# Performance work log

Hardware: AMD Instinct MI355X
Metric: run time of the kernel (lower is better)

The kernel has to match this reference:

```python
import jax, jax.numpy as jnp
import numpy as np

D_MODEL = 512
H = 8
DH = D_MODEL // H
P = H * (H - 1) // 2  # 28 head pairs
THRESH = 0.1
B, N = 2, 2048

# pair indices (i<j) in the same row-major order as the nested torch loop
_I_IDX, _J_IDX = np.triu_indices(H, k=1)
I_IDX = jnp.asarray(_I_IDX)
J_IDX = jnp.asarray(_J_IDX)


def setup_inputs() -> dict:
    key = jax.random.key(0)
    ks = jax.random.split(key, 10)
    s = 1.0 / np.sqrt(D_MODEL)
    return {
        "x": jax.random.normal(ks[0], (B, N, D_MODEL), dtype=jnp.float32),
        "Wq": jax.random.normal(ks[1], (D_MODEL, D_MODEL), dtype=jnp.float32) * s,
        "bq": jnp.zeros((D_MODEL,), dtype=jnp.float32),
        "Wk": jax.random.normal(ks[2], (D_MODEL, D_MODEL), dtype=jnp.float32) * s,
        "bk": jnp.zeros((D_MODEL,), dtype=jnp.float32),
        "Wv": jax.random.normal(ks[3], (D_MODEL, D_MODEL), dtype=jnp.float32) * s,
        "bv": jnp.zeros((D_MODEL,), dtype=jnp.float32),
        "Wo": jax.random.normal(ks[4], (D_MODEL, D_MODEL), dtype=jnp.float32) * s,
        "bo": jnp.zeros((D_MODEL,), dtype=jnp.float32),
        # stacked restriction maps: (P, DH_out, DH_in), Linear(bias=False)
        "Wr": jax.random.normal(ks[5], (P, DH, DH), dtype=jnp.float32) / np.sqrt(DH),
        "agreement_scale": jnp.asarray(1.0, dtype=jnp.float32),
    }


def reference(x, Wq, bq, Wk, bk, Wv, bv, Wo, bo, Wr, agreement_scale):
    b, n, d = x.shape
    # projections (torch Linear: y = x @ W.T + b), split into heads -> (B,H,N,DH)
    q = (x @ Wq.T + bq).reshape(b, n, H, DH).transpose(0, 2, 1, 3)
    k = (x @ Wk.T + bk).reshape(b, n, H, DH).transpose(0, 2, 1, 3)
    v = (x @ Wv.T + bv).reshape(b, n, H, DH).transpose(0, 2, 1, 3)

    scores = jnp.einsum("bhnd,bhmd->bhnm", q, k) / jnp.sqrt(jnp.asarray(DH, x.dtype))
    attn = jax.nn.softmax(scores, axis=-1)
    head_out = jnp.einsum("bhnm,bhmd->bhnd", attn, v)  # (B,H,N,DH)

    # --- pairwise restriction-map agreement, fully batched over the P pairs ---
    hi = head_out[:, I_IDX]  # (B,P,N,DH)
    hj = head_out[:, J_IDX]  # (B,P,N,DH)
    ri = jnp.einsum("bpnd,ped->bpne", hi, Wr)  # per-pair Linear(bias=False)
    diff = jnp.linalg.norm(ri - hj, axis=-1).mean(axis=-1)  # (B,P)
    score = jnp.exp(-diff * agreement_scale / THRESH)  # (B,P)

    agreement = jnp.zeros((b, H, H), dtype=x.dtype)
    agreement = agreement.at[:, I_IDX, J_IDX].set(score)
    agreement = agreement.at[:, J_IDX, I_IDX].set(score)
    diag = jnp.arange(H)
    agreement = agreement.at[:, diag, diag].set(1.0)

    # --- consensus aggregation ---
    offdiag = 1.0 - jnp.eye(H, dtype=x.dtype)
    consensus = (agreement * offdiag).sum(axis=-1) / (H - 1)  # (B,H)
    filtered = consensus * (consensus > THRESH).astype(x.dtype)
    weights = jax.nn.softmax(filtered + 1e-10, axis=-1)  # (B,H)

    agg = (head_out * weights[:, :, None, None]).sum(axis=1)  # (B,N,DH)
    agg = jnp.tile(agg, (1, 1, H))  # torch .repeat(1,1,H) -> (B,N,D)
    return agg @ Wo.T + bo
```

## Files before the change

### kernel.cpp

```cpp
#include <hip/hip_runtime.h>
#include <hip/hip_bf16.h>
#include <stdint.h>

typedef __attribute__((ext_vector_type(8))) short bf16x8;
typedef __attribute__((ext_vector_type(4))) float f32x4;
typedef __attribute__((ext_vector_type(4))) unsigned short u16x4;

#define LDS_SWZ(row, col) (((((col) >> 3) ^ ((row) & 7)) << 4))

__device__ __forceinline__ unsigned short f2bf(float f) {
  union { float f; unsigned u; } v; v.f = f;
  unsigned r = v.u + 0x7FFFu + ((v.u >> 16) & 1u);
  return (unsigned short)(r >> 16);
}
__device__ __forceinline__ float bf2f(unsigned short h) {
  union { unsigned u; float f; } v; v.u = ((unsigned)h) << 16;
  return v.f;
}
__device__ __forceinline__ unsigned pk2bf(float a, float b) {
  __hip_bfloat162 h2 = __float22bfloat162_rn(float2{a, b});
  unsigned u; __builtin_memcpy(&u, &h2, 4); return u;
}
__device__ __forceinline__ void gld_lds16(const void* g, void* l) {
  __builtin_amdgcn_global_load_lds((const __attribute__((address_space(1))) void*)g,
                                   (__attribute__((address_space(3))) void*)l, 16, 0, 0);
}

__global__ void k_prep(const float* __restrict__ x, const float* __restrict__ wq,
                       const float* __restrict__ wk, const float* __restrict__ wv,
                       const float* __restrict__ wr, const float* __restrict__ wo,
                       unsigned short* __restrict__ xb, unsigned short* __restrict__ wb,
                       unsigned short* __restrict__ wrb, unsigned short* __restrict__ wsb) {
  int q = blockIdx.x * blockDim.x + threadIdx.x;
  if (q >= 749568) {
    int t = q - 749568;
    if (t >= 512 * 64) return;
    int e = t >> 6, d = t & 63;
    float s = 0.f;
#pragma unroll
    for (int qq = 0; qq < 8; ++qq) s += wo[e * 512 + qq * 64 + d];
    wsb[t] = f2bf(s);
    return;
  }
  const float* src; unsigned short* dst; int off;
  if (q < 524288)      { src = x;  dst = xb;          off = q; }
  else if (q < 589824) { src = wq; dst = wb;          off = q - 524288; }
  else if (q < 655360) { src = wk; dst = wb + 262144; off = q - 589824; }
  else if (q < 720896) { src = wv; dst = wb + 524288; off = q - 655360; }
  else                 { src = wr; dst = wrb;         off = q - 720896; }
  float4 v = ((const float4*)src)[off];
  u16x4 o; o.x = f2bf(v.x); o.y = f2bf(v.y); o.z = f2bf(v.z); o.w = f2bf(v.w);
  ((u16x4*)dst)[off] = o;
}

__global__ __launch_bounds__(256) void k_qkv(
    const unsigned short* __restrict__ xb, const unsigned short* __restrict__ wb,
    const float* __restrict__ bq, const float* __restrict__ bk, const float* __restrict__ bv,
    unsigned short* __restrict__ qb, unsigned short* __restrict__ kb,
    unsigned short* __restrict__ vtb) {
  __shared__ alignas(16) unsigned char As[2][128 * 128];
  __shared__ alignas(16) unsigned char Bs[2][64 * 128];
  const int tid = threadIdx.x;
  const int wave = tid >> 6, lane = tid & 63;
  const int rowbase = blockIdx.x * 128;
  const int colbase = blockIdx.y * 64;
  const int z = blockIdx.z;
  const unsigned short* W = wb + z * 512 * 512;
  const float* bias = (z == 0) ? bq : ((z == 1) ? bk : bv);
  f32x4 acc[2][4] = {};

#define QKV_STAGE(buf, kt_)                                                            \
  do {                                                                                 \
    _Pragma("unroll") for (int i_ = 0; i_ < 4; ++i_) {                                 \
      const int L_ = i_ * 256 + tid;                                                   \
      const int row_ = L_ >> 3, pos_ = L_ & 7;                                         \
      gld_lds16(xb + (rowbase + row_) * 512 + (kt_) * 64 + ((pos_ ^ (row_ & 7)) << 3), \
                As[buf] + (i_ * 256 + wave * 64) * 16);                                \
    }                                                                                  \
    _Pragma("unroll") for (int i_ = 0; i_ < 2; ++i_) {                                 \
      const int L_ = i_ * 256 + tid;                                                   \
      const int row_ = L_ >> 3, pos_ = L_ & 7;                                         \
      gld_lds16(W + (colbase + row_) * 512 + (kt_) * 64 + ((pos_ ^ (row_ & 7)) << 3),  \
                Bs[buf] + (i_ * 256 + wave * 64) * 16);                                \
    }                                                                                  \
  } while (0)

  QKV_STAGE(0, 0);
  __syncthreads();
  for (int kt = 0; kt < 8; ++kt) {
    const int cur = kt & 1;
    if (kt < 7) QKV_STAGE(cur ^ 1, kt + 1);
#pragma unroll
    for (int kc = 0; kc < 2; ++kc) {
      bf16x8 af[2], bfr[4];
#pragma unroll
      for (int mq = 0; mq < 2; ++mq) {
        const int row = wave * 32 + mq * 16 + (lane & 15);
        const int col = kc * 32 + ((lane >> 4) << 3);
        af[mq] = *(const bf16x8*)(As[cur] + row * 128 + LDS_SWZ(row, col));
      }
#pragma unroll
      for (int nq = 0; nq < 4; ++nq) {
        const int row = nq * 16 + (lane & 15);
        const int col = kc * 32 + ((lane >> 4) << 3);
        bfr[nq] = *(const bf16x8*)(Bs[cur] + row * 128 + LDS_SWZ(row, col));
      }
#pragma unroll
      for (int mq = 0; mq < 2; ++mq)
#pragma unroll
        for (int nq = 0; nq < 4; ++nq)
          acc[mq][nq] = __builtin_amdgcn_mfma_f32_16x16x32_bf16(af[mq], bfr[nq], acc[mq][nq], 0, 0, 0);
    }
    __syncthreads();
  }
  const float qs = 0.18033688011112043f;
#pragma unroll
  for (int mq = 0; mq < 2; ++mq)
#pragma unroll
    for (int nq = 0; nq < 4; ++nq)
#pragma unroll
      for (int r = 0; r < 4; ++r) {
        const int grow = rowbase + wave * 32 + mq * 16 + ((lane >> 4) << 2) + r;
        const int col = colbase + nq * 16 + (lane & 15);
        float v = acc[mq][nq][r] + bias[col];
        const int b = grow >> 11, n = grow & 2047;
        const int h = col >> 6, dh = col & 63;
        if (z == 0)      qb[(((b << 3) + h) * 2048 + n) * 64 + dh] = f2bf(v * qs);
        else if (z == 1) kb[(((b << 3) + h) * 2048 + n) * 64 + dh] = f2bf(v);
        else             vtb[((((b << 3) + h) << 6) + dh) * 2048 + n] = f2bf(v);
      }
}

__global__ __launch_bounds__(512, 4) void k_attn(
    const unsigned short* __restrict__ qb, const unsigned short* __restrict__ kb,
    const unsigned short* __restrict__ vtb, unsigned short* __restrict__ hob) {
  __shared__ alignas(16) unsigned char smem[81920];
  const int tid = threadIdx.x, wave = tid >> 6, lane = tid & 63;
  const int team = wave >> 2, w4 = wave & 3;
  const int ttid = tid & 255;
  const int bid = blockIdx.x;
  const int bh = ((bid & 7) << 1) | ((bid >> 3) & 1);
  const int qt = bid >> 4;
  const int n0 = qt * 64 + w4 * 16;
  const int lq = lane & 15, lg = lane >> 4;
  unsigned char* Kt = smem + team * 32768;
  unsigned char* Vt = Kt + 16384;
  unsigned char* pw = smem + 65536 + wave * 2048;
  const unsigned short* kbase = kb + bh * 2048 * 64;
  const unsigned short* vbase = vtb + bh * 64 * 2048;
  bf16x8 qf[2];
#pragma unroll
  for (int kc = 0; kc < 2; ++kc)
    qf[kc] = *(const bf16x8*)(qb + (bh * 2048 + n0 + lq) * 64 + kc * 32 + (lg << 3));
  bf16x8 ones;
#pragma unroll
  for (int e = 0; e < 8; ++e) ones[e] = (short)0x3F80;
  f32x4 oacc[4] = {};
  f32x4 lacc = {};
  float mrun = -1e30f;

#define ATTN_STAGE(buf, T_)                                                        \
  do {                                                                             \
    _Pragma("unroll") for (int i_ = 0; i_ < 2; ++i_) {                             \
      const int L_ = i_ * 256 + ttid;                                              \
      const int row_ = L_ >> 3, pos_ = L_ & 7;                                     \
      gld_lds16(kbase + ((T_) * 64 + row_) * 64 + ((pos_ ^ (row_ & 7)) << 3),      \
                Kt + (buf) * 8192 + (i_ * 256 + w4 * 64) * 16);                    \
      gld_lds16(vbase + row_ * 2048 + (T_) * 64 + ((pos_ ^ (row_ & 7)) << 3),      \
                Vt + (buf) * 8192 + (i_ * 256 + w4 * 64) * 16);                    \
    }                                                                              \
  } while (0)

  ATTN_STAGE(0, team * 16);
  __syncthreads();
  for (int t = 0; t < 16; ++t) {
    const int cur = t & 1;
    if (t < 15) ATTN_STAGE(cur ^ 1, team * 16 + t + 1);
    f32x4 s[4];
    __builtin_amdgcn_s_setprio(1);
#pragma unroll
    for (int mc = 0; mc < 4; ++mc) {
      f32x4 zz = {};
#pragma unroll
      for (int kc = 0; kc < 2; ++kc) {
        const int row = mc * 16 + lq;
        const int col = kc * 32 + (lg << 3);
        bf16x8 kf = *(const bf16x8*)(Kt + cur * 8192 + row * 128 + LDS_SWZ(row, col));
        zz = __builtin_amdgcn_mfma_f32_16x16x32_bf16(kf, qf[kc], zz, 0, 0, 0);
      }
      s[mc] = zz;
    }
    __builtin_amdgcn_s_setprio(0);
    float t0 = fmaxf(fmaxf(s[0][0], s[0][1]), s[0][2]);
    float t1 = fmaxf(fmaxf(s[0][3], s[1][0]), s[1][1]);
    float t2 = fmaxf(fmaxf(s[1][2], s[1][3]), s[2][0]);
    float t3 = fmaxf(fmaxf(s[2][1], s[2][2]), s[2][3]);
    float t4 = fmaxf(fmaxf(s[3][0], s[3][1]), s[3][2]);
    float lm = fmaxf(fmaxf(fmaxf(t0, t1), t2), fmaxf(fmaxf(t3, t4), s[3][3]));
    if (__any(lm > mrun + 8.f)) {
      float v = fmaxf(lm, __shfl_xor(lm, 16));
      v = fmaxf(v, __shfl_xor(v, 32));
      float mnew = fmaxf(mrun, v);
      float sc = exp2f(mrun - mnew);
      mrun = mnew;
      float sco[4];
#pragma unroll
      for (int r = 0; r < 4; ++r) sco[r] = __shfl(sc, (lane & 48) | ((lg << 2) + r));
#pragma unroll
      for (int c2 = 0; c2 < 4; ++c2) {
        f32x4 o = oacc[c2];
#pragma unroll
        for (int r = 0; r < 4; ++r) o[r] *= sco[r];
        oacc[c2] = o;
      }
#pragma unroll
      for (int r = 0; r < 4; ++r) lacc[r] *= sco[r];
    }
#pragma unroll
    for (int mc = 0; mc < 4; ++mc) {
      float p0 = exp2f(s[mc][0] - mrun);
      float p1 = exp2f(s[mc][1] - mrun);
      float p2 = exp2f(s[mc][2] - mrun);
      float p3 = exp2f(s[mc][3] - mrun);
      *(uint2*)(pw + (mc * 4 + lg) * 128 + lq * 8) = uint2{pk2bf(p0, p1), pk2bf(p2, p3)};
    }
    bf16x8 pa[2];
#pragma unroll
    for (int kc = 0; kc < 2; ++kc) {
      uint2 a = *(const uint2*)(pw + (kc * 8 + lg * 2) * 128 + lq * 8);
      uint2 b = *(const uint2*)(pw + (kc * 8 + lg * 2 + 1) * 128 + lq * 8);
      union { uint4 u; bf16x8 v; } cv; cv.u = uint4{a.x, a.y, b.x, b.y};
      pa[kc] = cv.v;
    }
    __builtin_amdgcn_s_setprio(1);
    lacc = __builtin_amdgcn_mfma_f32_16x16x32_bf16(pa[0], ones, lacc, 0, 0, 0);
    lacc = __builtin_amdgcn_mfma_f32_16x16x32_bf16(pa[1], ones, lacc, 0, 0, 0);
#pragma unroll
    for (int c2 = 0; c2 < 4; ++c2) {
      f32x4 o = oacc[c2];
#pragma unroll
      for (int kc = 0; kc < 2; ++kc) {
        const int row = c2 * 16 + lq;
        const int col = kc * 32 + (lg << 3);
        bf16x8 vf = *(const bf16x8*)(Vt + cur * 8192 + row * 128 + LDS_SWZ(row, col));
        o = __builtin_amdgcn_mfma_f32_16x16x32_bf16(pa[kc], vf, o, 0, 0, 0);
      }
      oacc[c2] = o;
    }
    __builtin_amdgcn_s_setprio(0);
    __syncthreads();
  }
  float m_o[4];
#pragma unroll
  for (int r = 0; r < 4; ++r) m_o[r] = __shfl(mrun, (lane & 48) | ((lg << 2) + r));
  float* ex = (float*)smem;
  float* px = ex + (w4 * 64 + lane) * 25;
  if (team == 1) {
#pragma unroll
    for (int c2 = 0; c2 < 4; ++c2)
#pragma unroll
      for (int r = 0; r < 4; ++r) px[c2 * 4 + r] = oacc[c2][r];
#pragma unroll
    for (int r = 0; r < 4; ++r) { px[16 + r] = m_o[r]; px[20 + r] = lacc[r]; }
  }
  __syncthreads();
  if (team == 0) {
    float w0[4], w1[4];
#pragma unroll
    for (int r = 0; r < 4; ++r) {
      float m1 = px[16 + r], l1 = px[20 + r];
      float ms = fmaxf(m_o[r], m1);
      float a = exp2f(m_o[r] - ms), b = exp2f(m1 - ms);
      float li = 1.f / (a * lacc[r] + b * l1);
      w0[r] = a * li; w1[r] = b * li;
    }
#pragma unroll
    for (int c2 = 0; c2 < 4; ++c2)
#pragma unroll
      for (int r = 0; r < 4; ++r) {
        const int n = n0 + (lg << 2) + r;
        const int dh = c2 * 16 + lq;
        float o1 = px[c2 * 4 + r];
        hob[(bh * 2048 + n) * 64 + dh] = f2bf(w0[r] * oacc[c2][r] + w1[r] * o1);
      }
  }
}

__global__ __launch_bounds__(256) void k_pair(const unsigned short* __restrict__ hob,
                                              const unsigned short* __restrict__ wrb,
                                              float* __restrict__ dpart) {
  __shared__ alignas(16) unsigned char Ws[64 * 128];
  __shared__ alignas(16) unsigned char Hj[2][64 * 128];
  __shared__ float red[4];
  const int tid = threadIdx.x, wave = tid >> 6, lane = tid & 63;
  const int chunk = blockIdx.x & 7, bp = blockIdx.x >> 3;
  const int b = bp / 28, p = bp % 28;
  int pp = p, ii = 0;
  while (pp >= 7 - ii) { pp -= 7 - ii; ii++; }
  const int i = ii, j = ii + 1 + pp;
  const unsigned short* hib = hob + ((b * 8 + i) * 2048) * 64;
  const unsigned short* hjb = hob + ((b * 8 + j) * 2048) * 64;

#define PAIR_STAGE(buf, t_)                                                      \
  do {                                                                           \
    _Pragma("unroll") for (int is_ = 0; is_ < 2; ++is_) {                        \
      const int L_ = is_ * 256 + tid;                                            \
      const int row_ = L_ >> 3, pos_ = L_ & 7;                                   \
      gld_lds16(hjb + ((t_) * 64 + row_) * 64 + ((pos_ ^ (row_ & 7)) << 3),      \
                Hj[buf] + (is_ * 256 + wave * 64) * 16);                         \
    }                                                                            \
  } while (0)

#pragma unroll
  for (int is = 0; is < 2; ++is) {
    const int L = is * 256 + tid;
    const int row = L >> 3, pos = L & 7;
    gld_lds16(wrb + (p * 64 + row) * 64 + ((pos ^ (row & 7)) << 3), Ws + (is * 256 + wave * 64) * 16);
  }
  PAIR_STAGE(0, chunk * 4);
  __syncthreads();
  bf16x8 wf[4][2];
#pragma unroll
  for (int c = 0; c < 4; ++c)
#pragma unroll
    for (int kc = 0; kc < 2; ++kc) {
      const int row = c * 16 + (lane & 15);
      const int col = kc * 32 + ((lane >> 4) << 3);
      wf[c][kc] = *(const bf16x8*)(Ws + row * 128 + LDS_SWZ(row, col));
    }
  float wacc = 0.f;
  for (int t = 0; t < 4; ++t) {
    const int tt = chunk * 4 + t;
    const int cur = t & 1;
    if (t < 3) PAIR_STAGE(cur ^ 1, tt + 1);
    const int rbase = tt * 64 + wave * 16;
    f32x4 ri[4] = {};
#pragma unroll
    for (int kc = 0; kc < 2; ++kc) {
      bf16x8 hf = *(const bf16x8*)(hib + (rbase + (lane & 15)) * 64 + kc * 32 + ((lane >> 4) << 3));
#pragma unroll
      for (int c = 0; c < 4; ++c)
        ri[c] = __builtin_amdgcn_mfma_f32_16x16x32_bf16(hf, wf[c][kc], ri[c], 0, 0, 0);
    }
#pragma unroll
    for (int r = 0; r < 4; ++r) {
      const int row = wave * 16 + ((lane >> 4) << 2) + r;
      float ss = 0.f;
#pragma unroll
      for (int c = 0; c < 4; ++c) {
        const int col = c * 16 + (lane & 15);
        float hv = bf2f(*(const unsigned short*)(Hj[cur] + (row & 63) * 128 + LDS_SWZ(row & 63, col) + ((col & 7) << 1)));
        float d = ri[c][r] - hv;
        ss += d * d;
      }
#pragma unroll
      for (int off = 1; off < 16; off <<= 1) ss += __shfl_xor(ss, off);
      if ((lane & 15) == 0) wacc += sqrtf(ss);
    }
    __syncthreads();
  }
  float tot = __shfl(wacc, 0) + __shfl(wacc, 16) + __shfl(wacc, 32) + __shfl(wacc, 48);
  if (lane == 0) red[wave] = tot;
  __syncthreads();
  if (tid == 0) dpart[blockIdx.x] = red[0] + red[1] + red[2] + red[3];
}

__global__ __launch_bounds__(256) void k_agg(const unsigned short* __restrict__ hob,
                                             const float* __restrict__ dpart,
                                             const float* __restrict__ scal,
                                             unsigned short* __restrict__ aggb) {
  __shared__ float sc_s[2][28];
  __shared__ float filt[2][8];
  __shared__ float wts_s[16];
  const int tid = threadIdx.x;
  if (tid < 56) {
    int bb = tid / 28, pp = tid % 28;
    int base = (bb * 28 + pp) * 8;
    float diff = 0.f;
#pragma unroll
    for (int c = 0; c < 8; ++c) diff += dpart[base + c];
    diff /= 2048.f;
    sc_s[bb][pp] = expf(-diff * scal[0] / 0.1f);
  }
  __syncthreads();
  if (tid < 16) {
    int bb = tid / 8, h = tid % 8;
    float cons = 0.f;
    for (int h2 = 0; h2 < 8; ++h2)
      if (h2 != h) {
        int i_ = h < h2 ? h : h2, j_ = h < h2 ? h2 : h;
        int pp = i_ * (15 - i_) / 2 + (j_ - i_ - 1);
        cons += sc_s[bb][pp];
      }
    cons /= 7.f;
    filt[bb][h] = (cons > 0.1f) ? cons : 0.f;
  }
  __syncthreads();
  if (tid < 16) {
    int bb = tid / 8, h = tid % 8;
    float m = -1e30f;
    for (int h2 = 0; h2 < 8; ++h2) m = fmaxf(m, filt[bb][h2] + 1e-10f);
    float s = 0.f;
    for (int h2 = 0; h2 < 8; ++h2) s += expf(filt[bb][h2] + 1e-10f - m);
    wts_s[tid] = expf(filt[bb][h] + 1e-10f - m) / s;
  }
  __syncthreads();
  int t = blockIdx.x * blockDim.x + tid;
  if (t >= 4096 * 8) return;
  int r = t >> 3, dblk = t & 7;
  int b = r >> 11, n = r & 2047;
  float acc[8] = {};
#pragma unroll
  for (int h = 0; h < 8; ++h) {
    float w = wts_s[b * 8 + h];
    bf16x8 v = *(const bf16x8*)(hob + (((b * 8 + h) << 11) + n) * 64 + dblk * 8);
#pragma unroll
    for (int e = 0; e < 8; ++e) acc[e] += w * bf2f((unsigned short)v[e]);
  }
  bf16x8 o;
#pragma unroll
  for (int e = 0; e < 8; ++e) o[e] = (short)f2bf(acc[e]);
  *(bf16x8*)(aggb + r * 64 + dblk * 8) = o;
}

__global__ __launch_bounds__(256) void k_out(const unsigned short* __restrict__ aggb,
                                             const unsigned short* __restrict__ wsb,
                                             const float* __restrict__ bo,
                                             float* __restrict__ out) {
  __shared__ alignas(16) unsigned char Ws[64 * 128];
  const int tid = threadIdx.x, wave = tid >> 6, lane = tid & 63;
  const int rowb = blockIdx.x * 64, colb = blockIdx.y * 64;
#pragma unroll
  for (int is = 0; is < 2; ++is) {
    const int L = is * 256 + tid;
    const int row = L >> 3, pos = L & 7;
    gld_lds16(wsb + (colb + row) * 64 + ((pos ^ (row & 7)) << 3), Ws + (is * 256 + wave * 64) * 16);
  }
  __syncthreads();
  bf16x8 af[2];
#pragma unroll
  for (int kc = 0; kc < 2; ++kc)
    af[kc] = *(const bf16x8*)(aggb + (rowb + wave * 16 + (lane & 15)) * 64 + kc * 32 + ((lane >> 4) << 3));
  f32x4 acc[4] = {};
#pragma unroll
  for (int c = 0; c < 4; ++c)
#pragma unroll
    for (int kc = 0; kc < 2; ++kc) {
      const int row = c * 16 + (lane & 15);
      const int col = kc * 32 + ((lane >> 4) << 3);
      bf16x8 wfr = *(const bf16x8*)(Ws + row * 128 + LDS_SWZ(row, col));
      acc[c] = __builtin_amdgcn_mfma_f32_16x16x32_bf16(af[kc], wfr, acc[c], 0, 0, 0);
    }
#pragma unroll
  for (int c = 0; c < 4; ++c)
#pragma unroll
    for (int r = 0; r < 4; ++r) {
      const int grow = rowb + wave * 16 + ((lane >> 4) << 2) + r;
      const int col = colb + c * 16 + (lane & 15);
      out[grow * 512 + col] = acc[c][r] + bo[col];
    }
}

extern "C" void kernel_launch(void* const* d_in, const int* in_sizes, int n_in,
                              void* d_out, int out_size, void* d_ws, size_t ws_size,
                              hipStream_t stream) {
  const float* x  = (const float*)d_in[0];
  const float* Wq = (const float*)d_in[1];
  const float* bq = (const float*)d_in[2];
  const float* Wk = (const float*)d_in[3];
  const float* bk = (const float*)d_in[4];
  const float* Wv = (const float*)d_in[5];
  const float* bv = (const float*)d_in[6];
  const float* Wo = (const float*)d_in[7];
  const float* bo = (const float*)d_in[8];
  const float* Wr = (const float*)d_in[9];
  const float* ascale = (const float*)d_in[10];
  float* out = (float*)d_out;

  char* ws = (char*)d_ws;
  unsigned short* xb   = (unsigned short*)(ws);
  unsigned short* qb   = (unsigned short*)(ws + (4u << 20));
  unsigned short* kb   = (unsigned short*)(ws + (8u << 20));
  unsigned short* vtb  = (unsigned short*)(ws + (12u << 20));
  unsigned short* hob  = (unsigned short*)(ws + (16u << 20));
  unsigned short* wb   = (unsigned short*)(ws + (20u << 20));
  unsigned short* wrb  = (unsigned short*)(ws + (20u << 20) + 3u * 512 * 512 * 2);
  unsigned short* wsb  = (unsigned short*)(ws + (20u << 20) + 3u * 512 * 512 * 2 + 28u * 64 * 64 * 2);
  unsigned short* aggb = (unsigned short*)(ws + (22u << 20));
  float* dpart = (float*)(ws + (23u << 20));

  k_prep<<<3056, 256, 0, stream>>>(x, Wq, Wk, Wv, Wr, Wo, xb, wb, wrb, wsb);
  k_qkv<<<dim3(32, 8, 3), 256, 0, stream>>>(xb, wb, bq, bk, bv, qb, kb, vtb);
  k_attn<<<512, 512, 0, stream>>>(qb, kb, vtb, hob);
  k_pair<<<448, 256, 0, stream>>>(hob, wrb, dpart);
  k_agg<<<128, 256, 0, stream>>>(hob, dpart, ascale, aggb);
  k_out<<<dim3(64, 8), 256, 0, stream>>>(aggb, wsb, bo, out);
}
```

Measured before the change: 79.51 us.

## Split attention KV range across four waves per 16-query block, read K/V directly

Reworks the attention kernel so each 256-thread block handles 16 queries, with each of its four waves covering a quarter of the key range. K and V fragments are now read straight from global memory instead of being staged through double-buffered LDS, which removes the per-tile barriers. The four partial softmax states are then merged by a two-level tree reduction in shared memory. This adds parallelism and occupancy, but K/V reuse across query rows within a block is lost, so global/L2 traffic rises and loads are no longer overlapped by explicit prefetch.

```diff
diff --git a/kernel.cpp b/kernel.cpp
--- a/kernel.cpp
+++ b/kernel.cpp
@@ -131,21 +131,18 @@
       }
 }
 
-__global__ __launch_bounds__(512, 4) void k_attn(
+__global__ __launch_bounds__(256, 6) void k_attn(
     const unsigned short* __restrict__ qb, const unsigned short* __restrict__ kb,
     const unsigned short* __restrict__ vtb, unsigned short* __restrict__ hob) {
-  __shared__ alignas(16) unsigned char smem[81920];
+  __shared__ alignas(16) unsigned char smem[21504];
   const int tid = threadIdx.x, wave = tid >> 6, lane = tid & 63;
-  const int team = wave >> 2, w4 = wave & 3;
-  const int ttid = tid & 255;
   const int bid = blockIdx.x;
   const int bh = ((bid & 7) << 1) | ((bid >> 3) & 1);
   const int qt = bid >> 4;
-  const int n0 = qt * 64 + w4 * 16;
+  const int n0 = qt * 16;
   const int lq = lane & 15, lg = lane >> 4;
-  unsigned char* Kt = smem + team * 32768;
-  unsigned char* Vt = Kt + 16384;
-  unsigned char* pw = smem + 65536 + wave * 2048;
+  unsigned char* pw = smem + wave * 2048;
+  float* ex = (float*)(smem + 8192);
   const unsigned short* kbase = kb + bh * 2048 * 64;
   const unsigned short* vbase = vtb + bh * 64 * 2048;
   bf16x8 qf[2];
@@ -159,23 +156,10 @@
   f32x4 lacc = {};
   float mrun = -1e30f;
 
-#define ATTN_STAGE(buf, T_)                                                        \
-  do {                                                                             \
-    _Pragma("unroll") for (int i_ = 0; i_ < 2; ++i_) {                             \
-      const int L_ = i_ * 256 + ttid;                                              \
-      const int row_ = L_ >> 3, pos_ = L_ & 7;                                     \
-      gld_lds16(kbase + ((T_) * 64 + row_) * 64 + ((pos_ ^ (row_ & 7)) << 3),      \
-                Kt + (buf) * 8192 + (i_ * 256 + w4 * 64) * 16);                    \
-      gld_lds16(vbase + row_ * 2048 + (T_) * 64 + ((pos_ ^ (row_ & 7)) << 3),      \
-                Vt + (buf) * 8192 + (i_ * 256 + w4 * 64) * 16);                    \
-    }                                                                              \
-  } while (0)
-
-  ATTN_STAGE(0, team * 16);
-  __syncthreads();
-  for (int t = 0; t < 16; ++t) {
-    const int cur = t & 1;
-    if (t < 15) ATTN_STAGE(cur ^ 1, team * 16 + t + 1);
+  for (int t = 0; t < 8; ++t) {
+    const int T = wave * 8 + t;
+    const unsigned short* kt = kbase + T * 64 * 64;
+    const unsigned short* vt = vbase + T * 64;
     f32x4 s[4];
     __builtin_amdgcn_s_setprio(1);
 #pragma unroll
@@ -183,9 +167,7 @@
       f32x4 zz = {};
 #pragma unroll
       for (int kc = 0; kc < 2; ++kc) {
-        const int row = mc * 16 + lq;
-        const int col = kc * 32 + (lg << 3);
-        bf16x8 kf = *(const bf16x8*)(Kt + cur * 8192 + row * 128 + LDS_SWZ(row, col));
+        bf16x8 kf = *(const bf16x8*)(kt + (mc * 16 + lq) * 64 + kc * 32 + (lg << 3));
         zz = __builtin_amdgcn_mfma_f32_16x16x32_bf16(kf, qf[kc], zz, 0, 0, 0);
       }
       s[mc] = zz;
@@ -240,22 +222,18 @@
       f32x4 o = oacc[c2];
 #pragma unroll
       for (int kc = 0; kc < 2; ++kc) {
-        const int row = c2 * 16 + lq;
-        const int col = kc * 32 + (lg << 3);
-        bf16x8 vf = *(const bf16x8*)(Vt + cur * 8192 + row * 128 + LDS_SWZ(row, col));
+        bf16x8 vf = *(const bf16x8*)(vt + (c2 * 16 + lq) * 2048 + kc * 32 + (lg << 3));
         o = __builtin_amdgcn_mfma_f32_16x16x32_bf16(pa[kc], vf, o, 0, 0, 0);
       }
       oacc[c2] = o;
     }
     __builtin_amdgcn_s_setprio(0);
-    __syncthreads();
   }
   float m_o[4];
 #pragma unroll
   for (int r = 0; r < 4; ++r) m_o[r] = __shfl(mrun, (lane & 48) | ((lg << 2) + r));
-  float* ex = (float*)smem;
-  float* px = ex + (w4 * 64 + lane) * 25;
-  if (team == 1) {
+  if (wave & 1) {
+    float* px = ex + ((wave >> 1) * 64 + lane) * 25;
 #pragma unroll
     for (int c2 = 0; c2 < 4; ++c2)
 #pragma unroll
@@ -264,16 +242,46 @@
     for (int r = 0; r < 4; ++r) { px[16 + r] = m_o[r]; px[20 + r] = lacc[r]; }
   }
   __syncthreads();
-  if (team == 0) {
-    float w0[4], w1[4];
+  if (!(wave & 1)) {
+    float* px = ex + ((wave >> 1) * 64 + lane) * 25;
+    float aa[4], bb[4];
 #pragma unroll
     for (int r = 0; r < 4; ++r) {
       float m1 = px[16 + r], l1 = px[20 + r];
       float ms = fmaxf(m_o[r], m1);
-      float a = exp2f(m_o[r] - ms), b = exp2f(m1 - ms);
-      float li = 1.f / (a * lacc[r] + b * l1);
-      w0[r] = a * li; w1[r] = b * li;
-    }
+      aa[r] = exp2f(m_o[r] - ms); bb[r] = exp2f(m1 - ms);
+      m_o[r] = ms; lacc[r] = aa[r] * lacc[r] + bb[r] * l1;
+    }
+#pragma unroll
+    for (int c2 = 0; c2 < 4; ++c2)
+#pragma unroll
+      for (int r = 0; r < 4; ++r)
+        oacc[c2][r] = aa[r] * oacc[c2][r] + bb[r] * px[c2 * 4 + r];
+  }
+  __syncthreads();
+  if (wave == 2) {
+    float* px = ex + lane * 25;
+#pragma unroll
+    for (int c2 = 0; c2 < 4; ++c2)
+#pragma unroll
+      for (int r = 0; r < 4; ++r) px[c2 * 4 + r] = oacc[c2][r];
+#pragma unroll
+    for (int r = 0; r < 4; ++r) { px[16 + r] = m_o[r]; px[20 + r] = lacc[r]; }
+  }
+  __syncthreads();
+  if (wave == 0) {
+    float* px = ex + lane * 25;
+    float aa[4], bb[4];
+#pragma unroll
+    for (int r = 0; r < 4; ++r) {
+      float m1 = px[16 + r], l1 = px[20 + r];
+      float ms = fmaxf(m_o[r], m1);
+      aa[r] = exp2f(m_o[r] - ms); bb[r] = exp2f(m1 - ms);
+      lacc[r] = aa[r] * lacc[r] + bb[r] * l1;
+    }
+    float li[4];
+#pragma unroll
+    for (int r = 0; r < 4; ++r) li[r] = 1.f / lacc[r];
 #pragma unroll
     for (int c2 = 0; c2 < 4; ++c2)
 #pragma unroll
@@ -281,7 +289,7 @@
         const int n = n0 + (lg << 2) + r;
         const int dh = c2 * 16 + lq;
         float o1 = px[c2 * 4 + r];
-        hob[(bh * 2048 + n) * 64 + dh] = f2bf(w0[r] * oacc[c2][r] + w1[r] * o1);
+        hob[(bh * 2048 + n) * 64 + dh] = f2bf((aa[r] * oacc[c2][r] + bb[r] * o1) * li[r]);
       }
   }
 }
@@ -491,7 +499,7 @@
 
   k_prep<<<3056, 256, 0, stream>>>(x, Wq, Wk, Wv, Wr, Wo, xb, wb, wrb, wsb);
   k_qkv<<<dim3(32, 8, 3), 256, 0, stream>>>(xb, wb, bq, bk, bv, qb, kb, vtb);
-  k_attn<<<512, 512, 0, stream>>>(qb, kb, vtb, hob);
+  k_attn<<<2048, 256, 0, stream>>>(qb, kb, vtb, hob);
   k_pair<<<448, 256, 0, stream>>>(hob, wrb, dpart);
   k_agg<<<128, 256, 0, stream>>>(hob, dpart, ascale, aggb);
   k_out<<<dim3(64, 8), 256, 0, stream>>>(aggb, wsb, bo, out);
```

Result: slower. 160.0 us (+101.2%).

## Load V fragments directly from global in attention and fuse aggregation into output GEMM

Applied to the files above, without the earlier changes.

The attention kernel stops staging V tiles through LDS. Each wave now reads its V MFMA fragments straight from global memory, which cuts shared memory from 80KB to 48KB and raises the occupancy hint. Separately, the head-weighted aggregation kernel is merged into the output projection kernel, removing one launch and the round trip through the aggb buffer. The trade-offs are uncoalesced, latency-exposed global reads for V, and the aggregation being recomputed by each of the 8 column blocks.

```diff
diff --git a/kernel.cpp b/kernel.cpp
--- a/kernel.cpp
+++ b/kernel.cpp
@@ -131,10 +131,10 @@
       }
 }
 
-__global__ __launch_bounds__(512, 4) void k_attn(
+__global__ __launch_bounds__(512, 6) void k_attn(
     const unsigned short* __restrict__ qb, const unsigned short* __restrict__ kb,
     const unsigned short* __restrict__ vtb, unsigned short* __restrict__ hob) {
-  __shared__ alignas(16) unsigned char smem[81920];
+  __shared__ alignas(16) unsigned char smem[49152];
   const int tid = threadIdx.x, wave = tid >> 6, lane = tid & 63;
   const int team = wave >> 2, w4 = wave & 3;
   const int ttid = tid & 255;
@@ -143,9 +143,8 @@
   const int qt = bid >> 4;
   const int n0 = qt * 64 + w4 * 16;
   const int lq = lane & 15, lg = lane >> 4;
-  unsigned char* Kt = smem + team * 32768;
-  unsigned char* Vt = Kt + 16384;
-  unsigned char* pw = smem + 65536 + wave * 2048;
+  unsigned char* Kt = smem + team * 16384;
+  unsigned char* pw = smem + 32768 + wave * 2048;
   const unsigned short* kbase = kb + bh * 2048 * 64;
   const unsigned short* vbase = vtb + bh * 64 * 2048;
   bf16x8 qf[2];
@@ -159,23 +158,23 @@
   f32x4 lacc = {};
   float mrun = -1e30f;
 
-#define ATTN_STAGE(buf, T_)                                                        \
+#define ATTN_STAGE_K(buf, T_)                                                      \
   do {                                                                             \
     _Pragma("unroll") for (int i_ = 0; i_ < 2; ++i_) {                             \
       const int L_ = i_ * 256 + ttid;                                              \
       const int row_ = L_ >> 3, pos_ = L_ & 7;                                     \
       gld_lds16(kbase + ((T_) * 64 + row_) * 64 + ((pos_ ^ (row_ & 7)) << 3),      \
                 Kt + (buf) * 8192 + (i_ * 256 + w4 * 64) * 16);                    \
-      gld_lds16(vbase + row_ * 2048 + (T_) * 64 + ((pos_ ^ (row_ & 7)) << 3),      \
-                Vt + (buf) * 8192 + (i_ * 256 + w4 * 64) * 16);                    \
     }                                                                              \
   } while (0)
 
-  ATTN_STAGE(0, team * 16);
+  ATTN_STAGE_K(0, team * 16);
   __syncthreads();
   for (int t = 0; t < 16; ++t) {
     const int cur = t & 1;
-    if (t < 15) ATTN_STAGE(cur ^ 1, team * 16 + t + 1);
+    const int T = team * 16 + t;
+    const unsigned short* vt = vbase + T * 64;
+    if (t < 15) ATTN_STAGE_K(cur ^ 1, T + 1);
     f32x4 s[4];
     __builtin_amdgcn_s_setprio(1);
 #pragma unroll
@@ -224,6 +223,12 @@
       float p3 = exp2f(s[mc][3] - mrun);
       *(uint2*)(pw + (mc * 4 + lg) * 128 + lq * 8) = uint2{pk2bf(p0, p1), pk2bf(p2, p3)};
     }
+    bf16x8 vf[4][2];
+#pragma unroll
+    for (int c2 = 0; c2 < 4; ++c2)
+#pragma unroll
+      for (int kc = 0; kc < 2; ++kc)
+        vf[c2][kc] = *(const bf16x8*)(vt + (c2 * 16 + lq) * 2048 + kc * 32 + (lg << 3));
     bf16x8 pa[2];
 #pragma unroll
     for (int kc = 0; kc < 2; ++kc) {
@@ -239,12 +244,8 @@
     for (int c2 = 0; c2 < 4; ++c2) {
       f32x4 o = oacc[c2];
 #pragma unroll
-      for (int kc = 0; kc < 2; ++kc) {
-        const int row = c2 * 16 + lq;
-        const int col = kc * 32 + (lg << 3);
-        bf16x8 vf = *(const bf16x8*)(Vt + cur * 8192 + row * 128 + LDS_SWZ(row, col));
-        o = __builtin_amdgcn_mfma_f32_16x16x32_bf16(pa[kc], vf, o, 0, 0, 0);
-      }
+      for (int kc = 0; kc < 2; ++kc)
+        o = __builtin_amdgcn_mfma_f32_16x16x32_bf16(pa[kc], vf[c2][kc], o, 0, 0, 0);
       oacc[c2] = o;
     }
     __builtin_amdgcn_s_setprio(0);
@@ -365,14 +366,25 @@
   if (tid == 0) dpart[blockIdx.x] = red[0] + red[1] + red[2] + red[3];
 }
 
-__global__ __launch_bounds__(256) void k_agg(const unsigned short* __restrict__ hob,
+__global__ __launch_bounds__(256) void k_out(const unsigned short* __restrict__ hob,
                                              const float* __restrict__ dpart,
                                              const float* __restrict__ scal,
-                                             unsigned short* __restrict__ aggb) {
+                                             const unsigned short* __restrict__ wsb,
+                                             const float* __restrict__ bo,
+                                             float* __restrict__ out) {
+  __shared__ alignas(16) unsigned char Ws[64 * 128];
   __shared__ float sc_s[2][28];
   __shared__ float filt[2][8];
   __shared__ float wts_s[16];
-  const int tid = threadIdx.x;
+  const int tid = threadIdx.x, wave = tid >> 6, lane = tid & 63;
+  const int rowb = blockIdx.x * 64, colb = blockIdx.y * 64;
+  const int lq = lane & 15, lg = lane >> 4;
+#pragma unroll
+  for (int is = 0; is < 2; ++is) {
+    const int L = is * 256 + tid;
+    const int row = L >> 3, pos = L & 7;
+    gld_lds16(wsb + (colb + row) * 64 + ((pos ^ (row & 7)) << 3), Ws + (is * 256 + wave * 64) * 16);
+  }
   if (tid < 56) {
     int bb = tid / 28, pp = tid % 28;
     int base = (bb * 28 + pp) * 8;
@@ -405,58 +417,40 @@
     wts_s[tid] = expf(filt[bb][h] + 1e-10f - m) / s;
   }
   __syncthreads();
-  int t = blockIdx.x * blockDim.x + tid;
-  if (t >= 4096 * 8) return;
-  int r = t >> 3, dblk = t & 7;
-  int b = r >> 11, n = r & 2047;
-  float acc[8] = {};
-#pragma unroll
-  for (int h = 0; h < 8; ++h) {
-    float w = wts_s[b * 8 + h];
-    bf16x8 v = *(const bf16x8*)(hob + (((b * 8 + h) << 11) + n) * 64 + dblk * 8);
-#pragma unroll
-    for (int e = 0; e < 8; ++e) acc[e] += w * bf2f((unsigned short)v[e]);
-  }
-  bf16x8 o;
-#pragma unroll
-  for (int e = 0; e < 8; ++e) o[e] = (short)f2bf(acc[e]);
-  *(bf16x8*)(aggb + r * 64 + dblk * 8) = o;
-}
-
-__global__ __launch_bounds__(256) void k_out(const unsigned short* __restrict__ aggb,
-                                             const unsigned short* __restrict__ wsb,
-                                             const float* __restrict__ bo,
-                                             float* __restrict__ out) {
-  __shared__ alignas(16) unsigned char Ws[64 * 128];
-  const int tid = threadIdx.x, wave = tid >> 6, lane = tid & 63;
-  const int rowb = blockIdx.x * 64, colb = blockIdx.y * 64;
-#pragma unroll
-  for (int is = 0; is < 2; ++is) {
-    const int L = is * 256 + tid;
-    const int row = L >> 3, pos = L & 7;
-    gld_lds16(wsb + (colb + row) * 64 + ((pos ^ (row & 7)) << 3), Ws + (is * 256 + wave * 64) * 16);
-  }
-  __syncthreads();
+  const int row = rowb + wave * 16 + lq;
+  const int b = row >> 11, n = row & 2047;
   bf16x8 af[2];
 #pragma unroll
-  for (int kc = 0; kc < 2; ++kc)
-    af[kc] = *(const bf16x8*)(aggb + (rowb + wave * 16 + (lane & 15)) * 64 + kc * 32 + ((lane >> 4) << 3));
+  for (int kc = 0; kc < 2; ++kc) {
+    float facc[8] = {};
+#pragma unroll
+    for (int h = 0; h < 8; ++h) {
+      float w = wts_s[b * 8 + h];
+      bf16x8 v = *(const bf16x8*)(hob + (((b * 8 + h) * 2048) + n) * 64 + kc * 32 + (lg << 3));
+#pragma unroll
+      for (int e = 0; e < 8; ++e) facc[e] += w * bf2f((unsigned short)v[e]);
+    }
+    union { uint4 u; bf16x8 v; } cv;
+    cv.u = uint4{pk2bf(facc[0], facc[1]), pk2bf(facc[2], facc[3]),
+                 pk2bf(facc[4], facc[5]), pk2bf(facc[6], facc[7])};
+    af[kc] = cv.v;
+  }
   f32x4 acc[4] = {};
 #pragma unroll
   for (int c = 0; c < 4; ++c)
 #pragma unroll
     for (int kc = 0; kc < 2; ++kc) {
-      const int row = c * 16 + (lane & 15);
-      const int col = kc * 32 + ((lane >> 4) << 3);
-      bf16x8 wfr = *(const bf16x8*)(Ws + row * 128 + LDS_SWZ(row, col));
+      const int wrow = c * 16 + lq;
+      const int col = kc * 32 + (lg << 3);
+      bf16x8 wfr = *(const bf16x8*)(Ws + wrow * 128 + LDS_SWZ(wrow, col));
       acc[c] = __builtin_amdgcn_mfma_f32_16x16x32_bf16(af[kc], wfr, acc[c], 0, 0, 0);
     }
 #pragma unroll
   for (int c = 0; c < 4; ++c)
 #pragma unroll
     for (int r = 0; r < 4; ++r) {
-      const int grow = rowb + wave * 16 + ((lane >> 4) << 2) + r;
-      const int col = colb + c * 16 + (lane & 15);
+      const int grow = rowb + wave * 16 + (lg << 2) + r;
+      const int col = colb + c * 16 + lq;
       out[grow * 512 + col] = acc[c][r] + bo[col];
     }
 }
@@ -486,13 +480,11 @@
   unsigned short* wb   = (unsigned short*)(ws + (20u << 20));
   unsigned short* wrb  = (unsigned short*)(ws + (20u << 20) + 3u * 512 * 512 * 2);
   unsigned short* wsb  = (unsigned short*)(ws + (20u << 20) + 3u * 512 * 512 * 2 + 28u * 64 * 64 * 2);
-  unsigned short* aggb = (unsigned short*)(ws + (22u << 20));
   float* dpart = (float*)(ws + (23u << 20));
 
   k_prep<<<3056, 256, 0, stream>>>(x, Wq, Wk, Wv, Wr, Wo, xb, wb, wrb, wsb);
   k_qkv<<<dim3(32, 8, 3), 256, 0, stream>>>(xb, wb, bq, bk, bv, qb, kb, vtb);
   k_attn<<<512, 512, 0, stream>>>(qb, kb, vtb, hob);
   k_pair<<<448, 256, 0, stream>>>(hob, wrb, dpart);
-  k_agg<<<128, 256, 0, stream>>>(hob, dpart, ascale, aggb);
-  k_out<<<dim3(64, 8), 256, 0, stream>>>(aggb, wsb, bo, out);
-}
+  k_out<<<dim3(64, 8), 256, 0, stream>>>(hob, dpart, ascale, wsb, bo, out);
+}
```

New measurement: 120.6 us. +51.7%, slower.
